# Kernel tuning notes

Measured on AMD Instinct MI355X. Metric: run time of the kernel, lower is better.

The kernel has to match this reference:

```python
import jax, jax.numpy as jnp
import numpy as np

N, E, H, D, L, R = 50000, 800000, 128, 512, 3, 3
BN_EPS = 1e-5


def setup_inputs() -> dict:
    key = jax.random.key(0)
    ks = jax.random.split(key, 10)
    x = jax.random.normal(ks[0], (N, H), jnp.float32)
    edge_src = jax.random.randint(ks[1], (R, E), 0, N, jnp.int32)
    edge_dst = jax.random.randint(ks[2], (R, E), 0, N, jnp.int32)
    conv_W = jax.random.normal(ks[3], (L, R, H, H), jnp.float32) * 0.05
    conv_b = jnp.zeros((L, R, H), jnp.float32)
    fc_W = jax.random.normal(ks[4], (L - 1, H, H), jnp.float32) * 0.05
    fc_b = jnp.zeros((L - 1, H), jnp.float32)
    fc_W_last = jax.random.normal(ks[5], (H, D), jnp.float32) * 0.05
    fc_b_last = jnp.zeros((D,), jnp.float32)
    bn_gamma = jnp.ones((L - 1, H), jnp.float32)
    bn_beta = jnp.zeros((L - 1, H), jnp.float32)
    bn_mean = jax.random.normal(ks[6], (L - 1, H), jnp.float32) * 0.1
    bn_var = jax.random.uniform(ks[7], (L - 1, H), jnp.float32, 0.5, 1.5)
    return {"x": x, "edge_src": edge_src, "edge_dst": edge_dst,
            "conv_W": conv_W, "conv_b": conv_b, "fc_W": fc_W, "fc_b": fc_b,
            "fc_W_last": fc_W_last, "fc_b_last": fc_b_last,
            "bn_gamma": bn_gamma, "bn_beta": bn_beta,
            "bn_mean": bn_mean, "bn_var": bn_var}


def _deg_norm(idx, n, dtype):
    # symmetric GCN norm: 1/sqrt(clamp(deg,1))  (DGL norm='both')
    deg = jax.ops.segment_sum(jnp.ones(idx.shape, dtype), idx, num_segments=n)
    return jax.lax.rsqrt(jnp.maximum(deg, 1.0))


def reference(x, edge_src, edge_dst, conv_W, conv_b, fc_W, fc_b,
              fc_W_last, fc_b_last, bn_gamma, bn_beta, bn_mean, bn_var):
    n = x.shape[0]
    # per-relation degree norms (graph fixed across layers)
    norm_out = [_deg_norm(edge_src[r], n, x.dtype) for r in range(R)]  # src side
    norm_in = [_deg_norm(edge_dst[r], n, x.dtype) for r in range(R)]   # dst side

    for l in range(L):
        # HeteroGraphConv: sum of 3 relation-wise GraphConvs
        h = jnp.zeros((n, conv_W.shape[-1]), x.dtype)
        for r in range(R):
            m = (x * norm_out[r][:, None]) @ conv_W[l, r]          # [N,H] transform first
            agg = jax.ops.segment_sum(m[edge_src[r]], edge_dst[r], num_segments=n)
            h = h + agg * norm_in[r][:, None] + conv_b[l, r]
        if l != L - 1:
            x = h @ fc_W[l] + fc_b[l]
            x = jax.nn.relu(x)
            # BatchNorm1d in eval mode (running stats); dropout = identity in eval
            x = bn_gamma[l] * (x - bn_mean[l]) * jax.lax.rsqrt(bn_var[l] + BN_EPS) + bn_beta[l]
        else:
            x = h @ fc_W_last + fc_b_last
    return x
```

## Files before the change

kernel.cpp:

```cpp
#include <hip/hip_runtime.h>

#define NN 50000
#define EE 800000
#define RR 3
#define HH 128
#define CAP 64
#define NB 128
#define BW 391
#define NBLK 1172
#define SCB 32
#define OVCAP 4096

typedef __attribute__((ext_vector_type(8))) short short8;
typedef __attribute__((ext_vector_type(4))) float f32x4;
typedef unsigned short u16;
typedef unsigned int u32;
typedef unsigned long long u64;

__device__ __forceinline__ float b2f(u16 u){
  unsigned v = ((unsigned)u) << 16;
  return __builtin_bit_cast(float, v);
}
__device__ __forceinline__ u16 f2bu(float f){
  unsigned u = __builtin_bit_cast(unsigned, f);
  u += 0x7fffu + ((u >> 16) & 1u);
  return (u16)(u >> 16);
}

__global__ __launch_bounds__(128) void init_k(u32* __restrict__ xb32, u32* __restrict__ act32){
  int i = threadIdx.x;
  if (i < 64) xb32[(size_t)NN * 64 + i] = 0;
  else act32[(size_t)NN * 64 + (i - 64)] = 0;
}

__global__ __launch_bounds__(256) void bucket_p1(const int* __restrict__ src, const int* __restrict__ dst,
                                                 u32* __restrict__ bktd, u16* __restrict__ bkts,
                                                 int* __restrict__ cnt_d, int* __restrict__ cnt_s,
                                                 u64* __restrict__ ovd, u32* __restrict__ ovs,
                                                 int* __restrict__ ovcur){
  __shared__ int hd[RR * NB];
  __shared__ int hs[RR * NB];
  int tid = threadIdx.x, blk = blockIdx.x;
  for (int k = tid; k < RR * NB; k += 256){ hd[k] = 0; hs[k] = 0; }
  __syncthreads();

  int e0 = (blk * 256 + tid) * 8;
  if (e0 < RR * EE){
    int r = e0 / EE;
#pragma unroll
    for (int h = 0; h < 2; ++h){
      int4 s4 = ((const int4*)src)[(e0 >> 2) + h];
      int4 d4 = ((const int4*)dst)[(e0 >> 2) + h];
      int ss[4] = {s4.x, s4.y, s4.z, s4.w};
      int dd[4] = {d4.x, d4.y, d4.z, d4.w};
#pragma unroll
      for (int j = 0; j < 4; ++j){
        int bd = dd[j] / BW;
        int kd = r * NB + bd;
        u32 sv = (u32)ss[j] | ((u32)(dd[j] - bd * BW) << 16);
        int rk = atomicAdd(&hd[kd], 1);
        if (rk < SCB)
          bktd[((size_t)kd * NBLK + blk) * SCB + rk] = sv;
        else {
          int p = atomicAdd(&ovcur[0], 1);
          if (p < OVCAP) ovd[p] = ((u64)kd << 32) | (u64)sv;
        }
        int bs = ss[j] / BW;
        int ks = r * NB + bs;
        u16 sloc = (u16)(ss[j] - bs * BW);
        int rs = atomicAdd(&hs[ks], 1);
        if (rs < SCB)
          bkts[((size_t)ks * NBLK + blk) * SCB + rs] = sloc;
        else {
          int p = atomicAdd(&ovcur[1], 1);
          if (p < OVCAP) ovs[p] = ((u32)ks << 16) | (u32)sloc;
        }
      }
    }
  }
  __syncthreads();
  for (int k = tid; k < RR * NB; k += 256){
    cnt_d[blk * (RR * NB) + k] = hd[k];
    cnt_s[blk * (RR * NB) + k] = hs[k];
  }
}

__global__ __launch_bounds__(256) void slots_p2(const int* __restrict__ cnt_d, const u32* __restrict__ bktd,
                                                const u64* __restrict__ ovd, const int* __restrict__ ovcur,
                                                u16* __restrict__ slots, int* __restrict__ cnt_in){
  __shared__ int cur[BW];
  int k = blockIdx.x, tid = threadIdx.x;
  int r = k / NB, b = k % NB, d0 = b * BW;
  for (int i = tid; i < BW; i += 256) cur[i] = 0;
  __syncthreads();
  for (int blk = tid; blk < NBLK; blk += 256){
    int c = cnt_d[blk * (RR * NB) + k]; if (c > SCB) c = SCB;
    const u32* buf = bktd + ((size_t)k * NBLK + blk) * SCB;
    for (int t = 0; t < c; ++t){
      u32 pl = buf[t];
      int dl = (int)(pl >> 16), s = (int)(pl & 0xffffu);
      int p = atomicAdd(&cur[dl], 1);
      if (p < CAP) slots[((size_t)r * NN + d0 + dl) * CAP + p] = (u16)s;
    }
  }
  int nov = ovcur[0]; if (nov > OVCAP) nov = OVCAP;
  for (int t = tid; t < nov; t += 256){
    u64 e = ovd[t];
    if ((int)(e >> 32) == k){
      u32 pl = (u32)e;
      int dl = (int)(pl >> 16), s = (int)(pl & 0xffffu);
      int p = atomicAdd(&cur[dl], 1);
      if (p < CAP) slots[((size_t)r * NN + d0 + dl) * CAP + p] = (u16)s;
    }
  }
  __syncthreads();
  for (int i = tid; i < BW; i += 256){
    int d = d0 + i;
    if (d < NN) cnt_in[r * NN + d] = cur[i];
  }
}

__global__ __launch_bounds__(256) void hist_p2(const int* __restrict__ cnt_s, const u16* __restrict__ bkts,
                                               const u32* __restrict__ ovs, const int* __restrict__ ovcur,
                                               float* __restrict__ nout){
  __shared__ int cur[BW];
  int k = blockIdx.x, tid = threadIdx.x;
  int r = k / NB, b = k % NB, d0 = b * BW;
  for (int i = tid; i < BW; i += 256) cur[i] = 0;
  __syncthreads();
  for (int blk = tid; blk < NBLK; blk += 256){
    int c = cnt_s[blk * (RR * NB) + k]; if (c > SCB) c = SCB;
    const u16* buf = bkts + ((size_t)k * NBLK + blk) * SCB;
    for (int t = 0; t < c; ++t)
      atomicAdd(&cur[buf[t]], 1);
  }
  int nov = ovcur[1]; if (nov > OVCAP) nov = OVCAP;
  for (int t = tid; t < nov; t += 256){
    u32 e = ovs[t];
    if ((int)(e >> 16) == k)
      atomicAdd(&cur[e & 0xffffu], 1);
  }
  __syncthreads();
  for (int i = tid; i < BW; i += 256){
    int s = d0 + i;
    if (s < NN){
      int c = cur[i]; if (c < 1) c = 1;
      nout[r * NN + s] = rsqrtf((float)c);
    }
  }
}

__global__ __launch_bounds__(256) void norms2_k(const int* __restrict__ cin,
                                                float* __restrict__ nin, float* __restrict__ nout,
                                                u16* __restrict__ slots){
  int i = blockIdx.x * 256 + threadIdx.x;
  if (i >= RR * NN) return;
  int a = cin[i];
  int c = a; if (c > CAP) c = CAP;
  int n8 = (c + 7) & ~7;
  u16* sl = slots + (size_t)i * CAP;
  for (int p = c; p < n8; ++p) sl[p] = (u16)NN;
  if (a < 1) a = 1;
  nin[i] = rsqrtf((float)a);
  if (i == 0) nout[RR * NN] = 1.0f;
}

__global__ __launch_bounds__(256) void cvt_bf16(const float* __restrict__ in, u16* __restrict__ out, int n4){
  int i = blockIdx.x * 256 + threadIdx.x;
  if (i >= n4) return;
  float4 v = ((const float4*)in)[i];
  ushort4 o; o.x = f2bu(v.x); o.y = f2bu(v.y); o.z = f2bu(v.z); o.w = f2bu(v.w);
  ((ushort4*)out)[i] = o;
}

__global__ __launch_bounds__(256) void mergew(const float* __restrict__ convW, const float* __restrict__ fcW,
                                              const float* __restrict__ fcWl,
                                              u16* __restrict__ Wm01, u16* __restrict__ Wm2){
  int i = blockIdx.x * 256 + threadIdx.x;
  const int N01 = 2 * RR * 128 * 128;
  if (i < N01){
    int l = i / (RR * 128 * 128), rem = i % (RR * 128 * 128);
    int r = rem / (128 * 128), kc = rem % (128 * 128);
    int k = kc / 128, c = kc % 128;
    const float* A = convW + (((size_t)l * RR + r) * 128 + k) * 128;
    const float* B = fcW + (size_t)l * 128 * 128 + c;
    float s = 0.f;
#pragma unroll 4
    for (int t = 0; t < 128; ++t) s += A[t] * B[(size_t)t * 128];
    Wm01[((size_t)l * RR + r) * 128 * 128 + ((size_t)(k >> 3) * 128 + c) * 8 + (k & 7)] = f2bu(s);
  } else if (i < N01 + RR * 128 * 512){
    int j = i - N01;
    int r = j / (128 * 512), kc = j % (128 * 512);
    int k = kc / 512, c = kc % 512;
    const float* A = convW + (((size_t)2 * RR + r) * 128 + k) * 128;
    const float* B = fcWl + c;
    float s = 0.f;
#pragma unroll 4
    for (int t = 0; t < 128; ++t) s += A[t] * B[(size_t)t * 512];
    Wm2[(size_t)r * 128 * 512 + ((size_t)(k >> 3) * 512 + c) * 8 + (k & 7)] = f2bu(s);
  }
}

__global__ __launch_bounds__(256) void mergeb(const float* __restrict__ convB, const float* __restrict__ fcW,
                                              const float* __restrict__ fcB, const float* __restrict__ fcWl,
                                              const float* __restrict__ fcBl, float* __restrict__ bm){
  int i = blockIdx.x * 256 + threadIdx.x;
  if (i < 256){
    int l = i >> 7, c = i & 127;
    float s = fcB[l * 128 + c];
    for (int t = 0; t < 128; ++t){
      float bs = convB[(l * RR + 0) * 128 + t] + convB[(l * RR + 1) * 128 + t] + convB[(l * RR + 2) * 128 + t];
      s += bs * fcW[(size_t)l * 128 * 128 + (size_t)t * 128 + c];
    }
    bm[i] = s;
  } else if (i < 768){
    int c = i - 256;
    float s = fcBl[c];
    for (int t = 0; t < 128; ++t){
      float bs = convB[(2 * RR + 0) * 128 + t] + convB[(2 * RR + 1) * 128 + t] + convB[(2 * RR + 2) * 128 + t];
      s += bs * fcWl[(size_t)t * 512 + c];
    }
    bm[i] = s;
  }
}

__global__ __launch_bounds__(256) void gather_agg(
    const u16* __restrict__ xin, const u16* __restrict__ slots,
    const int* __restrict__ cin, const float* __restrict__ nin,
    const float* __restrict__ nout, u16* __restrict__ agg)
{
  int tid = threadIdx.x;
  int lane = tid & 63;
  int ql = lane & 15;
  int qb = lane & 48;
  int r = blockIdx.y;
  int row = blockIdx.x * 16 + (tid >> 4);
  int rNN = r * NN;
  const u16* sl = slots + ((size_t)rNN + row) * CAP;
  int cnt = cin[rNN + row]; if (cnt > CAP) cnt = CAP;
  int n8 = (cnt + 7) & ~7;
  float a[8];
#pragma unroll
  for (int k = 0; k < 8; ++k) a[k] = 0.f;

  u32 w = (u32)sl[ql];
  for (int base = 0; base < n8; base += 16){
    u32 wn = 0u;
    if (base + 16 < n8) wn = (u32)sl[base + 16 + ql];
#pragma unroll
    for (int gstep = 0; gstep < 16; gstep += 8){
      if (base + gstep < n8){
        int uu[8]; float cf[8]; short8 vv[8];
#pragma unroll
        for (int j = 0; j < 8; ++j)
          uu[j] = __shfl((int)w, qb + gstep + j);
#pragma unroll
        for (int j = 0; j < 8; ++j)
          vv[j] = *(const short8*)(xin + (size_t)uu[j] * HH + ql * 8);
#pragma unroll
        for (int j = 0; j < 8; ++j)
          cf[j] = nout[rNN + uu[j]];
#pragma unroll
        for (int j = 0; j < 8; ++j){
          float c = cf[j];
#pragma unroll
          for (int k = 0; k < 8; ++k)
            a[k] += c * b2f((u16)vv[j][k]);
        }
      }
    }
    w = wn;
  }
  float sc = nin[rNN + row];
  short8 o;
#pragma unroll
  for (int k = 0; k < 8; ++k) o[k] = (short)f2bu(sc * a[k]);
  *(short8*)(agg + ((size_t)rNN + row) * HH + ql * 8) = o;
}

template<int MODE>
__global__ __launch_bounds__(256) void dense_m(
    const u16* __restrict__ agg, const u16* __restrict__ Wm, const float* __restrict__ bm,
    const float* __restrict__ g, const float* __restrict__ be,
    const float* __restrict__ mu, const float* __restrict__ va,
    u16* __restrict__ out_bf, float* __restrict__ out_f)
{
  const int NC = MODE ? 512 : 128;
  __shared__ u16 tile[32][136];
  int tid = threadIdx.x, wave = tid >> 6, lane = tid & 63;
  int q = lane >> 4, l15 = lane & 15;
  int rh = wave & 1, ch = wave >> 1;
  int nb = blockIdx.x * 32;
  int cs = blockIdx.y;
  int cbase = cs * 128 + ch * 64;
  f32x4 zf = {0.f, 0.f, 0.f, 0.f};
  f32x4 acc[4];
#pragma unroll
  for (int ct = 0; ct < 4; ++ct) acc[ct] = zf;

  for (int r = 0; r < RR; ++r){
    if (r) __syncthreads();
#pragma unroll
    for (int p = 0; p < 2; ++p){
      int chunk = p * 256 + tid;
      int rw = chunk >> 4, cc = chunk & 15;
      int node = nb + rw;
      if (node >= NN) node = NN - 1;
      short8 v = *(const short8*)(agg + ((size_t)r * NN + node) * HH + cc * 8);
      *(short8*)&tile[rw][cc * 8] = v;
    }
    __syncthreads();
    const short8* bpr = (const short8*)(Wm + (size_t)r * HH * NC);
#pragma unroll
    for (int kb = 0; kb < 4; ++kb){
      short8 a = *(const short8*)&tile[rh * 16 + l15][kb * 32 + q * 8];
#pragma unroll
      for (int ct = 0; ct < 4; ++ct){
        short8 b = bpr[(kb * 4 + q) * NC + cbase + ct * 16 + l15];
        acc[ct] = __builtin_amdgcn_mfma_f32_16x16x32_bf16(a, b, acc[ct], 0, 0, 0);
      }
    }
  }

  if (MODE == 0){
#pragma unroll
    for (int ct = 0; ct < 4; ++ct){
      int col = cbase + ct * 16 + l15;
      float bb = bm[col];
      float s0 = g[col] * rsqrtf(va[col] + 1e-5f);
      float m0 = mu[col], b0 = be[col];
#pragma unroll
      for (int i = 0; i < 4; ++i){
        int node = nb + rh * 16 + q * 4 + i;
        if (node < NN){
          float v = acc[ct][i] + bb;
          v = fmaxf(v, 0.f);
          v = (v - m0) * s0 + b0;
          out_bf[(size_t)node * HH + col] = f2bu(v);
        }
      }
    }
  } else {
#pragma unroll
    for (int ct = 0; ct < 4; ++ct){
      int col = cbase + ct * 16 + l15;
      float bb = bm[col];
#pragma unroll
      for (int i = 0; i < 4; ++i){
        int node = nb + rh * 16 + q * 4 + i;
        if (node < NN) out_f[(size_t)node * 512 + col] = acc[ct][i] + bb;
      }
    }
  }
}

extern "C" void kernel_launch(void* const* d_in, const int* in_sizes, int n_in,
                              void* d_out, int out_size, void* d_ws, size_t ws_size,
                              hipStream_t stream){
  const float* x_in  = (const float*)d_in[0];
  const int* esrc    = (const int*)d_in[1];
  const int* edst    = (const int*)d_in[2];
  const float* convW = (const float*)d_in[3];
  const float* convB = (const float*)d_in[4];
  const float* fcW   = (const float*)d_in[5];
  const float* fcB   = (const float*)d_in[6];
  const float* fcWl  = (const float*)d_in[7];
  const float* fcBl  = (const float*)d_in[8];
  const float* bng   = (const float*)d_in[9];
  const float* bnb   = (const float*)d_in[10];
  const float* bnm   = (const float*)d_in[11];
  const float* bnv   = (const float*)d_in[12];

  char* w = (char*)d_ws;
  size_t off = 0;
  auto alloc = [&](size_t bytes) -> char* {
    char* p = w + off;
    off += (bytes + 255) & ~(size_t)255;
    return p;
  };
  size_t BKTD_B = (size_t)RR * NB * NBLK * SCB * 4;
  size_t BKTS_B = (size_t)RR * NB * NBLK * SCB * 2;
  size_t AGG_B  = (size_t)RR * NN * HH * 2;
  size_t XB_B   = (size_t)(NN + 1) * HH * 2;
  char* regionA = alloc(BKTD_B + BKTS_B);
  u32* bktd = (u32*)regionA;
  u16* bkts = (u16*)(regionA + BKTD_B);
  u16* agg  = (u16*)regionA;
  u16* xb   = (u16*)(regionA + ((AGG_B + 255) & ~(size_t)255));
  u16* act  = (u16*)(regionA + ((AGG_B + XB_B + 511) & ~(size_t)255));

  int* cnt_d   = (int*)alloc((size_t)NBLK * RR * NB * 4);
  int* cnt_s   = (int*)alloc((size_t)NBLK * RR * NB * 4);
  int* cnt_in  = (int*)alloc((size_t)RR * NN * 4);
  float* nin   = (float*)alloc((size_t)RR * NN * 4);
  float* nout  = (float*)alloc((size_t)(RR * NN + 1) * 4);
  u16* slots   = (u16*)alloc((size_t)RR * NN * CAP * 2);
  u64* ovd     = (u64*)alloc((size_t)OVCAP * 8);
  u32* ovs     = (u32*)alloc((size_t)OVCAP * 4);
  int* ovcur   = (int*)alloc(256);
  u16* Wm01    = (u16*)alloc((size_t)2 * RR * 128 * 128 * 2);
  u16* Wm2     = (u16*)alloc((size_t)RR * 128 * 512 * 2);
  float* bm    = (float*)alloc((size_t)768 * 4);

  const int TPB = 256;
  hipMemsetAsync(ovcur, 0, 8, stream);
  bucket_p1<<<NBLK, TPB, 0, stream>>>(esrc, edst, bktd, bkts, cnt_d, cnt_s, ovd, ovs, ovcur);
  slots_p2<<<RR * NB, TPB, 0, stream>>>(cnt_d, bktd, ovd, ovcur, slots, cnt_in);
  hist_p2<<<RR * NB, TPB, 0, stream>>>(cnt_s, bkts, ovs, ovcur, nout);
  norms2_k<<<(RR * NN + TPB - 1) / TPB, TPB, 0, stream>>>(cnt_in, nin, nout, slots);
  init_k<<<1, 128, 0, stream>>>((u32*)xb, (u32*)act);
  cvt_bf16<<<(NN * HH / 4 + TPB - 1) / TPB, TPB, 0, stream>>>(x_in, xb, NN * HH / 4);
  {
    int total = 2 * RR * 128 * 128 + RR * 128 * 512;
    mergew<<<(total + TPB - 1) / TPB, TPB, 0, stream>>>(convW, fcW, fcWl, Wm01, Wm2);
    mergeb<<<3, TPB, 0, stream>>>(convB, fcW, fcB, fcWl, fcBl, bm);
  }

  dim3 ggrid(NN / 16, RR);
  dim3 dgrid0((NN + 31) / 32, 1);
  dim3 dgrid1((NN + 31) / 32, 4);

  gather_agg<<<ggrid, TPB, 0, stream>>>(xb, slots, cnt_in, nin, nout, agg);
  dense_m<0><<<dgrid0, TPB, 0, stream>>>(agg, Wm01 + (size_t)0 * RR * 128 * 128, bm + 0,
      bng + 0 * 128, bnb + 0 * 128, bnm + 0 * 128, bnv + 0 * 128, act, nullptr);
  gather_agg<<<ggrid, TPB, 0, stream>>>(act, slots, cnt_in, nin, nout, agg);
  dense_m<0><<<dgrid0, TPB, 0, stream>>>(agg, Wm01 + (size_t)1 * RR * 128 * 128, bm + 128,
      bng + 1 * 128, bnb + 1 * 128, bnm + 1 * 128, bnv + 1 * 128, act, nullptr);
  gather_agg<<<ggrid, TPB, 0, stream>>>(act, slots, cnt_in, nin, nout, agg);
  dense_m<1><<<dgrid1, TPB, 0, stream>>>(agg, Wm2, bm + 256,
      nullptr, nullptr, nullptr, nullptr, nullptr, (float*)d_out);
}
```

Measured before the change: 576.1 us.

## Pre-scale activations by per-relation source norm instead of gathering norms per edge

The source-degree norm is no longer loaded per neighbour inside the gather. Instead, activations are stored as three bf16 copies, one per relation, each pre-multiplied by that relation's norm. The input conversion and each hidden dense epilogue write all three copies, and the gather becomes a plain sum. This removes the scattered per-edge norm loads and multiplies, at the cost of tripling activation writes and storage and reading three distinct source arrays.

New measurement: 597.5 us. +3.7%, slower.

```diff
diff --git a/kernel.cpp b/kernel.cpp
--- a/kernel.cpp
+++ b/kernel.cpp
@@ -25,12 +25,6 @@
   unsigned u = __builtin_bit_cast(unsigned, f);
   u += 0x7fffu + ((u >> 16) & 1u);
   return (u16)(u >> 16);
-}
-
-__global__ __launch_bounds__(128) void init_k(u32* __restrict__ xb32, u32* __restrict__ act32){
-  int i = threadIdx.x;
-  if (i < 64) xb32[(size_t)NN * 64 + i] = 0;
-  else act32[(size_t)NN * 64 + (i - 64)] = 0;
 }
 
 __global__ __launch_bounds__(256) void bucket_p1(const int* __restrict__ src, const int* __restrict__ dst,
@@ -151,8 +145,7 @@
 }
 
 __global__ __launch_bounds__(256) void norms2_k(const int* __restrict__ cin,
-                                                float* __restrict__ nin, float* __restrict__ nout,
-                                                u16* __restrict__ slots){
+                                                float* __restrict__ nin, u16* __restrict__ slots){
   int i = blockIdx.x * 256 + threadIdx.x;
   if (i >= RR * NN) return;
   int a = cin[i];
@@ -162,15 +155,32 @@
   for (int p = c; p < n8; ++p) sl[p] = (u16)NN;
   if (a < 1) a = 1;
   nin[i] = rsqrtf((float)a);
-  if (i == 0) nout[RR * NN] = 1.0f;
-}
-
-__global__ __launch_bounds__(256) void cvt_bf16(const float* __restrict__ in, u16* __restrict__ out, int n4){
+}
+
+__global__ __launch_bounds__(256) void scale3_k(const float* __restrict__ x_in, const float* __restrict__ nout,
+                                                u16* __restrict__ xs){
   int i = blockIdx.x * 256 + threadIdx.x;
-  if (i >= n4) return;
-  float4 v = ((const float4*)in)[i];
-  ushort4 o; o.x = f2bu(v.x); o.y = f2bu(v.y); o.z = f2bu(v.z); o.w = f2bu(v.w);
-  ((ushort4*)out)[i] = o;
+  const int total = NN * 16;
+  if (i < total){
+    int node = i >> 4, f = (i & 15) * 8;
+    const float* xp = x_in + (size_t)node * HH + f;
+    float4 v0 = *(const float4*)xp;
+    float4 v1 = *(const float4*)(xp + 4);
+#pragma unroll
+    for (int r = 0; r < RR; ++r){
+      float c = nout[r * NN + node];
+      short8 o;
+      o[0] = (short)f2bu(v0.x * c); o[1] = (short)f2bu(v0.y * c);
+      o[2] = (short)f2bu(v0.z * c); o[3] = (short)f2bu(v0.w * c);
+      o[4] = (short)f2bu(v1.x * c); o[5] = (short)f2bu(v1.y * c);
+      o[6] = (short)f2bu(v1.z * c); o[7] = (short)f2bu(v1.w * c);
+      *(short8*)(xs + ((size_t)r * (NN + 1) + node) * HH + f) = o;
+    }
+  } else if (i < total + 48){
+    int j = i - total; int r = j / 16, f = (j % 16) * 8;
+    short8 z = {0,0,0,0,0,0,0,0};
+    *(short8*)(xs + ((size_t)r * (NN + 1) + NN) * HH + f) = z;
+  }
 }
 
 __global__ __launch_bounds__(256) void mergew(const float* __restrict__ convW, const float* __restrict__ fcW,
@@ -225,9 +235,9 @@
 }
 
 __global__ __launch_bounds__(256) void gather_agg(
-    const u16* __restrict__ xin, const u16* __restrict__ slots,
+    const u16* __restrict__ xs, const u16* __restrict__ slots,
     const int* __restrict__ cin, const float* __restrict__ nin,
-    const float* __restrict__ nout, u16* __restrict__ agg)
+    u16* __restrict__ agg)
 {
   int tid = threadIdx.x;
   int lane = tid & 63;
@@ -236,6 +246,7 @@
   int r = blockIdx.y;
   int row = blockIdx.x * 16 + (tid >> 4);
   int rNN = r * NN;
+  const u16* xbase = xs + (size_t)r * (NN + 1) * HH;
   const u16* sl = slots + ((size_t)rNN + row) * CAP;
   int cnt = cin[rNN + row]; if (cnt > CAP) cnt = CAP;
   int n8 = (cnt + 7) & ~7;
@@ -250,22 +261,18 @@
 #pragma unroll
     for (int gstep = 0; gstep < 16; gstep += 8){
       if (base + gstep < n8){
-        int uu[8]; float cf[8]; short8 vv[8];
+        int uu[8]; short8 vv[8];
 #pragma unroll
         for (int j = 0; j < 8; ++j)
           uu[j] = __shfl((int)w, qb + gstep + j);
 #pragma unroll
         for (int j = 0; j < 8; ++j)
-          vv[j] = *(const short8*)(xin + (size_t)uu[j] * HH + ql * 8);
-#pragma unroll
-        for (int j = 0; j < 8; ++j)
-          cf[j] = nout[rNN + uu[j]];
+          vv[j] = *(const short8*)(xbase + (size_t)uu[j] * HH + ql * 8);
 #pragma unroll
         for (int j = 0; j < 8; ++j){
-          float c = cf[j];
 #pragma unroll
           for (int k = 0; k < 8; ++k)
-            a[k] += c * b2f((u16)vv[j][k]);
+            a[k] += b2f((u16)vv[j][k]);
         }
       }
     }
@@ -283,7 +290,7 @@
     const u16* __restrict__ agg, const u16* __restrict__ Wm, const float* __restrict__ bm,
     const float* __restrict__ g, const float* __restrict__ be,
     const float* __restrict__ mu, const float* __restrict__ va,
-    u16* __restrict__ out_bf, float* __restrict__ out_f)
+    const float* __restrict__ nout, u16* __restrict__ act_s, float* __restrict__ out_f)
 {
   const int NC = MODE ? 512 : 128;
   __shared__ u16 tile[32][136];
@@ -336,7 +343,9 @@
           float v = acc[ct][i] + bb;
           v = fmaxf(v, 0.f);
           v = (v - m0) * s0 + b0;
-          out_bf[(size_t)node * HH + col] = f2bu(v);
+#pragma unroll
+          for (int r2 = 0; r2 < RR; ++r2)
+            act_s[((size_t)r2 * (NN + 1) + node) * HH + col] = f2bu(v * nout[r2 * NN + node]);
         }
       }
     }
@@ -381,19 +390,19 @@
   size_t BKTD_B = (size_t)RR * NB * NBLK * SCB * 4;
   size_t BKTS_B = (size_t)RR * NB * NBLK * SCB * 2;
   size_t AGG_B  = (size_t)RR * NN * HH * 2;
-  size_t XB_B   = (size_t)(NN + 1) * HH * 2;
-  char* regionA = alloc(BKTD_B + BKTS_B);
+  size_t XS_B   = (size_t)RR * (NN + 1) * HH * 2;
+  size_t REGA   = BKTD_B + BKTS_B;
+  char* regionA = alloc(REGA);
   u32* bktd = (u32*)regionA;
   u16* bkts = (u16*)(regionA + BKTD_B);
   u16* agg  = (u16*)regionA;
-  u16* xb   = (u16*)(regionA + ((AGG_B + 255) & ~(size_t)255));
-  u16* act  = (u16*)(regionA + ((AGG_B + XB_B + 511) & ~(size_t)255));
+  u16* xs   = (u16*)(regionA + ((AGG_B + 255) & ~(size_t)255));
 
   int* cnt_d   = (int*)alloc((size_t)NBLK * RR * NB * 4);
   int* cnt_s   = (int*)alloc((size_t)NBLK * RR * NB * 4);
   int* cnt_in  = (int*)alloc((size_t)RR * NN * 4);
   float* nin   = (float*)alloc((size_t)RR * NN * 4);
-  float* nout  = (float*)alloc((size_t)(RR * NN + 1) * 4);
+  float* nout  = (float*)alloc((size_t)RR * NN * 4);
   u16* slots   = (u16*)alloc((size_t)RR * NN * CAP * 2);
   u64* ovd     = (u64*)alloc((size_t)OVCAP * 8);
   u32* ovs     = (u32*)alloc((size_t)OVCAP * 4);
@@ -407,9 +416,8 @@
   bucket_p1<<<NBLK, TPB, 0, stream>>>(esrc, edst, bktd, bkts, cnt_d, cnt_s, ovd, ovs, ovcur);
   slots_p2<<<RR * NB, TPB, 0, stream>>>(cnt_d, bktd, ovd, ovcur, slots, cnt_in);
   hist_p2<<<RR * NB, TPB, 0, stream>>>(cnt_s, bkts, ovs, ovcur, nout);
-  norms2_k<<<(RR * NN + TPB - 1) / TPB, TPB, 0, stream>>>(cnt_in, nin, nout, slots);
-  init_k<<<1, 128, 0, stream>>>((u32*)xb, (u32*)act);
-  cvt_bf16<<<(NN * HH / 4 + TPB - 1) / TPB, TPB, 0, stream>>>(x_in, xb, NN * HH / 4);
+  norms2_k<<<(RR * NN + TPB - 1) / TPB, TPB, 0, stream>>>(cnt_in, nin, slots);
+  scale3_k<<<(NN * 16 + 48 + TPB - 1) / TPB, TPB, 0, stream>>>(x_in, nout, xs);
   {
     int total = 2 * RR * 128 * 128 + RR * 128 * 512;
     mergew<<<(total + TPB - 1) / TPB, TPB, 0, stream>>>(convW, fcW, fcWl, Wm01, Wm2);
@@ -420,13 +428,13 @@
   dim3 dgrid0((NN + 31) / 32, 1);
   dim3 dgrid1((NN + 31) / 32, 4);
 
-  gather_agg<<<ggrid, TPB, 0, stream>>>(xb, slots, cnt_in, nin, nout, agg);
+  gather_agg<<<ggrid, TPB, 0, stream>>>(xs, slots, cnt_in, nin, agg);
   dense_m<0><<<dgrid0, TPB, 0, stream>>>(agg, Wm01 + (size_t)0 * RR * 128 * 128, bm + 0,
-      bng + 0 * 128, bnb + 0 * 128, bnm + 0 * 128, bnv + 0 * 128, act, nullptr);
-  gather_agg<<<ggrid, TPB, 0, stream>>>(act, slots, cnt_in, nin, nout, agg);
+      bng + 0 * 128, bnb + 0 * 128, bnm + 0 * 128, bnv + 0 * 128, nout, xs, nullptr);
+  gather_agg<<<ggrid, TPB, 0, stream>>>(xs, slots, cnt_in, nin, agg);
   dense_m<0><<<dgrid0, TPB, 0, stream>>>(agg, Wm01 + (size_t)1 * RR * 128 * 128, bm + 128,
-      bng + 1 * 128, bnb + 1 * 128, bnm + 1 * 128, bnv + 1 * 128, act, nullptr);
-  gather_agg<<<ggrid, TPB, 0, stream>>>(act, slots, cnt_in, nin, nout, agg);
+      bng + 1 * 128, bnb + 1 * 128, bnm + 1 * 128, bnv + 1 * 128, nout, xs, nullptr);
+  gather_agg<<<ggrid, TPB, 0, stream>>>(xs, slots, cnt_in, nin, agg);
   dense_m<1><<<dgrid1, TPB, 0, stream>>>(agg, Wm2, bm + 256,
-      nullptr, nullptr, nullptr, nullptr, nullptr, (float*)d_out);
-}
+      nullptr, nullptr, nullptr, nullptr, nullptr, nullptr, (float*)d_out);
+}
```
